# Kernel tuning notes

Hardware: AMD Instinct MI355X
Metric: run time of the kernel (lower is better)

The kernel has to match this reference:

```python
import jax, jax.numpy as jnp
import numpy as np

NLAT, NLON = 64, 64
CIN = 512
HEADS = 8


def _cc_weights(n):
    # Clenshaw-Curtis quadrature weights on [-1, 1] for nodes cos(k*pi/(n-1)),
    # as used by torch-harmonics for the 'equiangular' grid. Weights sum to 2.
    N = n - 1
    theta = np.pi * np.arange(n) / N
    m = N // 2
    j = np.arange(1, m + 1)
    b = np.where(2 * j == N, 1.0, 2.0)
    S = (b / (4.0 * j ** 2 - 1.0))[None, :] * np.cos(2.0 * j[None, :] * theta[:, None])
    w = 1.0 - S.sum(axis=1)
    c = np.full(n, 2.0)
    c[0] = 1.0
    c[-1] = 1.0
    return c * w / N


def _log_quad_weights(nlat, nlon):
    # _precompute_latitudes flips nodes/weights; then 2*pi*w/nlon tiled over lon.
    w = _cc_weights(nlat)[::-1].copy()
    qw = 2.0 * np.pi * w / nlon                       # (nlat,)
    qw = np.tile(qw[:, None], (1, nlon)).reshape(-1)  # (nlat*nlon,)
    return jnp.asarray(np.log(qw), dtype=jnp.float32)


def setup_inputs() -> dict:
    key = jax.random.key(0)
    ks = jax.random.split(key, 5)
    s_qkv = float(np.sqrt(3.0 / CIN))   # scale for q/k/v 1x1-conv weights
    s_proj = float(np.sqrt(3.0 / CIN))  # out_channels == CIN
    u = lambda k, sh, s: jax.random.uniform(k, sh, jnp.float32, -s, s)
    return dict(
        query=jax.random.normal(ks[0], (1, CIN, NLAT, NLON), jnp.float32),
        q_w=u(ks[1], (CIN, CIN), s_qkv), q_b=jnp.zeros((CIN,), jnp.float32),
        k_w=u(ks[2], (CIN, CIN), s_qkv), k_b=jnp.zeros((CIN,), jnp.float32),
        v_w=u(ks[3], (CIN, CIN), s_qkv), v_b=jnp.zeros((CIN,), jnp.float32),
        p_w=u(ks[4], (CIN, CIN), s_proj), p_b=jnp.zeros((CIN,), jnp.float32),
        log_quad_weights=_log_quad_weights(NLAT, NLON),
    )


def reference(query, q_w, q_b, k_w, k_b, v_w, v_b, p_w, p_b, log_quad_weights):
    B, C, H, W = query.shape
    hd = C // HEADS  # head dim (k_channels == out_channels == in_channels)

    def proj_tokens(x, w, b):
        # 1x1 conv == channel matmul, then split heads and flatten H*W tokens
        y = jnp.einsum('bihw,oi->bohw', x, w) + b[None, :, None, None]
        return y.reshape(B, HEADS, -1, H, W).transpose(0, 1, 3, 4, 2).reshape(B, HEADS, H * W, -1)

    q = proj_tokens(query, q_w, q_b)  # (B, heads, HW, hd)
    k = proj_tokens(query, k_w, k_b)  # self-attention: key/value default to query
    v = proj_tokens(query, v_w, v_b)

    scale = 1.0 / jnp.sqrt(jnp.asarray(hd, dtype=q.dtype))
    # additive log-quadrature bias over keys (broadcast over batch/head/query)
    logits = jnp.einsum('bhqd,bhkd->bhqk', q, k) * scale + log_quad_weights[None, None, None, :]
    attn = jax.nn.softmax(logits, axis=-1)
    out = jnp.einsum('bhqk,bhkd->bhqd', attn, v)          # (B, heads, HW, hd)
    out = out.transpose(0, 1, 3, 2).reshape(B, HEADS * hd, H, W)
    return jnp.einsum('bihw,oi->bohw', out, p_w) + p_b[None, :, None, None]
```

## Files before the change

kernel.cpp:

```cpp
#include <hip/hip_runtime.h>

typedef unsigned short u16;
typedef unsigned int u32;
typedef __bf16 bf16x8 __attribute__((ext_vector_type(8)));
typedef float f32x4 __attribute__((ext_vector_type(4)));
typedef unsigned short u16x4 __attribute__((ext_vector_type(4)));

#define LOG2E 1.4426950408889634f

#if __has_builtin(__builtin_amdgcn_exp2f)
#define EXP2F(x) __builtin_amdgcn_exp2f(x)
#else
#define EXP2F(x) exp2f(x)
#endif

__device__ __forceinline__ u16 f2bf(float f) {
    union { float f; u32 u; } a; a.f = f;
    u32 u = a.u;
    u += 0x7FFFu + ((u >> 16) & 1u);
    return (u16)(u >> 16);
}
__device__ __forceinline__ bf16x8 ldg8(const u16* p) {
    return *reinterpret_cast<const bf16x8*>(p);
}
#if __has_builtin(__builtin_amdgcn_cvt_pk_bf16_f32)
__device__ __forceinline__ u32 pack2(float a, float b) {
    auto r = __builtin_amdgcn_cvt_pk_bf16_f32(a, b);
    return __builtin_bit_cast(u32, r);
}
#else
__device__ __forceinline__ u32 pack2(float a, float b) {
    u32 ua = __float_as_uint(a) + 0x8000u;
    u32 ub = __float_as_uint(b) + 0x8000u;
    return __builtin_amdgcn_perm(ub, ua, 0x07060302);
}
#endif
__device__ __forceinline__ void async16(const void* g, void* l) {
    __builtin_amdgcn_global_load_lds(
        (const __attribute__((address_space(1))) u32*)g,
        (__attribute__((address_space(3))) u32*)l, 16, 0, 0);
}

#define MFMA16(a, b, c) __builtin_amdgcn_mfma_f32_16x16x32_bf16((a), (b), (c), 0, 0, 0)

__global__ __launch_bounds__(256) void prep(const float* __restrict__ X,
                                            u16* __restrict__ Xt,
                                            const float* __restrict__ s0,
                                            const float* __restrict__ s1,
                                            const float* __restrict__ s2,
                                            const float* __restrict__ s3,
                                            u16* __restrict__ Wqkv,
                                            u16* __restrict__ Wp,
                                            const float* __restrict__ lqw,
                                            float* __restrict__ lqw2g) {
    __shared__ u16 tile[64][65];
    const int tid = threadIdx.x;
    const int y = blockIdx.y;

    if (y < 8) {
        const int t0 = blockIdx.x * 64;
        const int c0 = y * 64;
#pragma unroll
        for (int i = 0; i < 16; ++i) {
            int idx = tid + i * 256;
            int r = idx >> 6, cc = idx & 63;
            tile[r][cc] = f2bf(X[(size_t)(c0 + r) * 4096 + t0 + cc]);
        }
        __syncthreads();
#pragma unroll
        for (int i = 0; i < 16; ++i) {
            int idx = tid + i * 256;
            int tr = idx >> 6, cc = idx & 63;
            Xt[(size_t)(t0 + tr) * 512 + c0 + cc] = tile[cc][tr];
        }
    } else if (y < 12) {
        const int m = y - 8;
        const float* s = (m == 0) ? s0 : (m == 1) ? s1 : (m == 2) ? s2 : s3;
        u16* d = (m == 3) ? Wp : Wqkv + (size_t)m * 262144;
#pragma unroll
        for (int j = 0; j < 4; ++j) {
            int i = blockIdx.x * 1024 + j * 256 + tid;
            float4 v = reinterpret_cast<const float4*>(s)[i];
            u16x4 o;
            o[0] = f2bf(v.x); o[1] = f2bf(v.y); o[2] = f2bf(v.z); o[3] = f2bf(v.w);
            reinterpret_cast<u16x4*>(d)[i] = o;
        }
    } else {
        if (blockIdx.x < 4) {
            int i = blockIdx.x * 256 + tid;
            float4 v = reinterpret_cast<const float4*>(lqw)[i];
            v.x *= LOG2E; v.y *= LOG2E; v.z *= LOG2E; v.w *= LOG2E;
            reinterpret_cast<float4*>(lqw2g)[i] = v;
        }
    }
}

__global__ __launch_bounds__(512, 2) void qkv_gemm(const u16* __restrict__ Wqkv,
                                                   const u16* __restrict__ Xt,
                                                   const float* __restrict__ qb,
                                                   const float* __restrict__ kb,
                                                   const float* __restrict__ vb,
                                                   u16* __restrict__ Qt,
                                                   u16* __restrict__ Kt,
                                                   u16* __restrict__ Vp) {
    __shared__ __align__(16) u16 Al[2][128 * 32];
    __shared__ __align__(16) u16 Bl[2][128 * 32];

    const int tid = threadIdx.x;
    const int w = tid >> 6, lane = tid & 63;
    const int quad = lane >> 4, lm = lane & 15;
    const int wm = w & 1, wn = w >> 1;
    const int n0 = blockIdx.x * 128;
    const int my = blockIdx.y;
    const int m0 = my * 128;

    const int arow = lane >> 2;
    const int sch = (lane & 3) ^ ((lane >> 3) & 3);
    const u16* agp = Wqkv + (size_t)(m0 + w * 16 + arow) * 512 + sch * 8;
    const u16* bgp = Xt + (size_t)(n0 + w * 16 + arow) * 512 + sch * 8;

    async16(agp, &Al[0][w * 16 * 32]);
    async16(bgp, &Bl[0][w * 16 * 32]);
    agp += 32; bgp += 32;

    const int FOFF = lm * 64 + ((quad ^ ((lm >> 1) & 3)) << 4);

    f32x4 acc[4][2];
#pragma unroll
    for (int mt = 0; mt < 4; ++mt)
#pragma unroll
        for (int bt = 0; bt < 2; ++bt) acc[mt][bt] = (f32x4){0.f, 0.f, 0.f, 0.f};

    __syncthreads();

    for (int s = 0; s < 16; ++s) {
        const int buf = s & 1;
        if (s < 15) {
            async16(agp, &Al[buf ^ 1][w * 16 * 32]);
            async16(bgp, &Bl[buf ^ 1][w * 16 * 32]);
            agp += 32; bgp += 32;
        }
        const char* Ab = (const char*)&Al[buf][0];
        const char* Bb = (const char*)&Bl[buf][0];
        bf16x8 af[4], bfr[2];
#pragma unroll
        for (int mt = 0; mt < 4; ++mt)
            af[mt] = *(const bf16x8*)(Ab + wm * 4096 + mt * 1024 + FOFF);
#pragma unroll
        for (int bt = 0; bt < 2; ++bt)
            bfr[bt] = *(const bf16x8*)(Bb + wn * 2048 + bt * 1024 + FOFF);
#pragma unroll
        for (int mt = 0; mt < 4; ++mt)
#pragma unroll
            for (int bt = 0; bt < 2; ++bt)
                acc[mt][bt] = MFMA16(af[mt], bfr[bt], acc[mt][bt]);
        __syncthreads();
    }

    const int mat = my >> 2;
    const float* bias = (mat == 0) ? qb : (mat == 1) ? kb : vb;
    const int chbase = (my & 3) * 128 + wm * 64 + quad * 4;

    if (mat < 2) {
        u16* out = mat ? Kt : Qt;
        const float sc = mat ? 1.0f : 0.125f * LOG2E;
#pragma unroll
        for (int mt = 0; mt < 4; ++mt) {
            const int ch = chbase + mt * 16;
            float4 bv = *(const float4*)(bias + ch);
            float bvf[4] = {bv.x, bv.y, bv.z, bv.w};
#pragma unroll
            for (int bt = 0; bt < 2; ++bt) {
                int tok = n0 + wn * 32 + bt * 16 + lm;
                u16x4 pk;
#pragma unroll
                for (int r = 0; r < 4; ++r)
                    pk[r] = f2bf((acc[mt][bt][r] + bvf[r]) * sc);
                *(u16x4*)(out + (size_t)tok * 512 + ch) = pk;
            }
        }
    } else {
#pragma unroll
        for (int mt = 0; mt < 4; ++mt) {
            const int ch = chbase + mt * 16;
            float4 bv = *(const float4*)(bias + ch);
            float bvf[4] = {bv.x, bv.y, bv.z, bv.w};
#pragma unroll
            for (int bt = 0; bt < 2; ++bt) {
                int g = bt * 16 + lm;
                int col = n0 + wn * 32 + 8 * ((g >> 2) & 3) + 4 * ((g >> 4) & 1) + (g & 3);
#pragma unroll
                for (int r = 0; r < 4; ++r)
                    Vp[(size_t)(ch + r) * 4096 + col] = f2bf(acc[mt][bt][r] + bvf[r]);
            }
        }
    }
}

__global__ __launch_bounds__(256, 2) void out_gemm(const u16* __restrict__ Wp,
                                                   const u16* __restrict__ Ot,
                                                   const float* __restrict__ pb,
                                                   float* __restrict__ out) {
    __shared__ __align__(16) u16 Al[2][128 * 32];
    __shared__ __align__(16) u16 Bl[2][64 * 32];

    const int tid = threadIdx.x;
    const int w = tid >> 6, lane = tid & 63;
    const int quad = lane >> 4, lm = lane & 15;
    const int wm = w & 1, wn = w >> 1;
    const int n0 = blockIdx.x * 64;
    const int m0 = blockIdx.y * 128;

    const int arow = lane >> 2;
    const int sch = (lane & 3) ^ ((lane >> 3) & 3);
    const u16* agp0 = Wp + (size_t)(m0 + w * 16 + arow) * 512 + sch * 8;
    const u16* agp1 = agp0 + (size_t)64 * 512;
    const u16* bgp = Ot + (size_t)(n0 + w * 16 + arow) * 512 + sch * 8;

    async16(agp0, &Al[0][w * 16 * 32]);
    async16(agp1, &Al[0][(64 + w * 16) * 32]);
    async16(bgp, &Bl[0][w * 16 * 32]);
    agp0 += 32; agp1 += 32; bgp += 32;

    const int FOFF = lm * 64 + ((quad ^ ((lm >> 1) & 3)) << 4);

    f32x4 acc[4][2];
#pragma unroll
    for (int mt = 0; mt < 4; ++mt)
#pragma unroll
        for (int bt = 0; bt < 2; ++bt) acc[mt][bt] = (f32x4){0.f, 0.f, 0.f, 0.f};

    __syncthreads();

    for (int s = 0; s < 16; ++s) {
        const int buf = s & 1;
        if (s < 15) {
            async16(agp0, &Al[buf ^ 1][w * 16 * 32]);
            async16(agp1, &Al[buf ^ 1][(64 + w * 16) * 32]);
            async16(bgp, &Bl[buf ^ 1][w * 16 * 32]);
            agp0 += 32; agp1 += 32; bgp += 32;
        }
        const char* Ab = (const char*)&Al[buf][0];
        const char* Bb = (const char*)&Bl[buf][0];
        bf16x8 af[4], bfr[2];
#pragma unroll
        for (int mt = 0; mt < 4; ++mt)
            af[mt] = *(const bf16x8*)(Ab + wm * 4096 + mt * 1024 + FOFF);
#pragma unroll
        for (int bt = 0; bt < 2; ++bt)
            bfr[bt] = *(const bf16x8*)(Bb + wn * 2048 + bt * 1024 + FOFF);
#pragma unroll
        for (int mt = 0; mt < 4; ++mt)
#pragma unroll
            for (int bt = 0; bt < 2; ++bt)
                acc[mt][bt] = MFMA16(af[mt], bfr[bt], acc[mt][bt]);
        __syncthreads();
    }

#pragma unroll
    for (int mt = 0; mt < 4; ++mt) {
        const int ch = m0 + wm * 64 + mt * 16 + quad * 4;
        float4 bv = *(const float4*)(pb + ch);
        float bvf[4] = {bv.x, bv.y, bv.z, bv.w};
#pragma unroll
        for (int bt = 0; bt < 2; ++bt) {
            int tok = n0 + wn * 32 + bt * 16 + lm;
#pragma unroll
            for (int r = 0; r < 4; ++r)
                out[(size_t)(ch + r) * 4096 + tok] = acc[mt][bt][r] + bvf[r];
        }
    }
}

#define WAITVM(N) asm volatile("s_waitcnt vmcnt(" #N ")" ::: "memory")

__global__ __launch_bounds__(256, 2) void flash_attn(const u16* __restrict__ Qt,
                                                     const u16* __restrict__ Kt,
                                                     const u16* __restrict__ Vp,
                                                     const float* __restrict__ lqw2g,
                                                     u16* __restrict__ Ot) {
    __shared__ __align__(16) char smem[65536];

    const int tid = threadIdx.x;
    const int w = tid >> 6, lane = tid & 63;
    const int quad = lane >> 4, lm = lane & 15;
    const int bid = blockIdx.x;
    const int h = bid & 7, hq = h * 64;
    const int q0 = (bid >> 3) * 64;
    const int kstart = w * 1024;

    char* kvw = smem + w * 8192;

    const int srow = lane >> 3;
    const int schunk = (lane & 7) ^ srow;
    const u16* kg = Kt + (size_t)(kstart + srow) * 512 + hq + schunk * 8;

    const u16* vp = Vp + (size_t)(hq + lm) * 4096 + kstart + quad * 8;

    bf16x8 bq0[4], bq1[4];
#pragma unroll
    for (int s = 0; s < 4; ++s) {
        const u16* qb = Qt + (size_t)(q0 + s * 16 + lm) * 512 + hq + quad * 8;
        bq0[s] = ldg8(qb);
        bq1[s] = ldg8(qb + 32);
    }

    f32x4 breg0 = *(const f32x4*)(lqw2g + kstart + quad * 4);
    f32x4 breg1 = *(const f32x4*)(lqw2g + kstart + 16 + quad * 4);
    const float* bptr = lqw2g + kstart + 32 + quad * 4;

    const int A0 = lm * 128 + ((quad ^ (lm & 7)) << 4);
    const int A1 = A0 ^ 64;

#define STAGEK(DST)                                                            \
    {                                                                          \
        char* nb = (DST);                                                      \
        async16(kg, nb);                                                       \
        async16(kg + 8 * 512, nb + 1024);                                      \
        async16(kg + 16 * 512, nb + 2048);                                     \
        async16(kg + 24 * 512, nb + 3072);                                     \
        kg += 32 * 512;                                                        \
    }

    STAGEK(kvw)
    STAGEK(kvw + 4096)

    union { u32 u[4]; bf16x8 v; } onesu;
    onesu.u[0] = onesu.u[1] = onesu.u[2] = onesu.u[3] = 0x3F803F80u;
    const bf16x8 onesv = onesu.v;

    f32x4 acc_o[4][4];
#pragma unroll
    for (int mt = 0; mt < 4; ++mt)
#pragma unroll
        for (int s = 0; s < 4; ++s) acc_o[mt][s] = (f32x4){0.f, 0.f, 0.f, 0.f};
    f32x4 acc_l[4];
#pragma unroll
    for (int s = 0; s < 4; ++s) acc_l[s] = (f32x4){0.f, 0.f, 0.f, 0.f};

    union { u32 u[4]; bf16x8 v; } pb_[4];
    bf16x8 pv0, pv1, pv2, pv3;
    int bufsel = 0;

#define BODY(WN, DOBIAS, DOSTAGE, DOPV)                                        \
    {                                                                          \
        WAITVM(WN);                                                            \
        bf16x8 nv0 = ldg8(vp);                                                 \
        bf16x8 nv1 = ldg8(vp + (size_t)16 * 4096);                             \
        bf16x8 nv2 = ldg8(vp + (size_t)32 * 4096);                             \
        bf16x8 nv3 = ldg8(vp + (size_t)48 * 4096);                             \
        vp += 32;                                                              \
        const char* Kb = kvw + bufsel;                                         \
        bf16x8 k00 = *(const bf16x8*)(Kb + A0);                                \
        bf16x8 k01 = *(const bf16x8*)(Kb + A1);                                \
        bf16x8 k10 = *(const bf16x8*)(Kb + 2048 + A0);                         \
        bf16x8 k11 = *(const bf16x8*)(Kb + 2048 + A1);                         \
        if (DOPV) {                                                            \
            _Pragma("unroll")                                                  \
            for (int s = 0; s < 4; ++s) {                                      \
                acc_o[0][s] = MFMA16(pv0, pb_[s].v, acc_o[0][s]);              \
                acc_o[1][s] = MFMA16(pv1, pb_[s].v, acc_o[1][s]);              \
                acc_o[2][s] = MFMA16(pv2, pb_[s].v, acc_o[2][s]);              \
                acc_o[3][s] = MFMA16(pv3, pb_[s].v, acc_o[3][s]);              \
                acc_l[s] = MFMA16(onesv, pb_[s].v, acc_l[s]);                  \
            }                                                                  \
        }                                                                      \
        _Pragma("unroll")                                                      \
        for (int s = 0; s < 4; ++s) {                                          \
            f32x4 a = MFMA16(k00, bq0[s], breg0);                              \
            a = MFMA16(k01, bq1[s], a);                                        \
            pb_[s].u[0] = pack2(EXP2F(a[0]), EXP2F(a[1]));                     \
            pb_[s].u[1] = pack2(EXP2F(a[2]), EXP2F(a[3]));                     \
        }                                                                      \
        _Pragma("unroll")                                                      \
        for (int s = 0; s < 4; ++s) {                                          \
            f32x4 c = MFMA16(k10, bq0[s], breg1);                              \
            c = MFMA16(k11, bq1[s], c);                                        \
            pb_[s].u[2] = pack2(EXP2F(c[0]), EXP2F(c[1]));                     \
            pb_[s].u[3] = pack2(EXP2F(c[2]), EXP2F(c[3]));                     \
        }                                                                      \
        if (DOBIAS) {                                                          \
            breg0 = *(const f32x4*)(bptr);                                     \
            breg1 = *(const f32x4*)(bptr + 16);                                \
            bptr += 32;                                                        \
        }                                                                      \
        pv0 = nv0; pv1 = nv1; pv2 = nv2; pv3 = nv3;                            \
        if (DOSTAGE) STAGEK(kvw + bufsel)                                      \
        bufsel ^= 4096;                                                        \
    }

    BODY(4, true, true, false)
    for (int t = 1; t < 30; ++t)
        BODY(10, true, true, true)
    BODY(10, true, false, true)
    BODY(6, false, false, true)

#undef BODY
#undef STAGEK

#pragma unroll
    for (int s = 0; s < 4; ++s) {
        acc_o[0][s] = MFMA16(pv0, pb_[s].v, acc_o[0][s]);
        acc_o[1][s] = MFMA16(pv1, pb_[s].v, acc_o[1][s]);
        acc_o[2][s] = MFMA16(pv2, pb_[s].v, acc_o[2][s]);
        acc_o[3][s] = MFMA16(pv3, pb_[s].v, acc_o[3][s]);
        acc_l[s] = MFMA16(onesv, pb_[s].v, acc_l[s]);
    }

    __syncthreads();
    float* mbuf = (float*)smem;
    if (w != 0) {
        float* ob = mbuf + (w - 1) * 4096;
#pragma unroll
        for (int s = 0; s < 4; ++s) {
            const int r = s * 16 + lm;
#pragma unroll
            for (int mt = 0; mt < 4; ++mt) {
                const int sl = (mt * 4 + quad) ^ lm;
                *(f32x4*)(ob + r * 64 + sl * 4) = acc_o[mt][s];
            }
        }
        if (quad == 0) {
#pragma unroll
            for (int s = 0; s < 4; ++s)
                mbuf[12288 + (w - 1) * 64 + s * 16 + lm] = acc_l[s][0];
        }
    }
    __syncthreads();
    if (w != 0) return;

#pragma unroll
    for (int s = 0; s < 4; ++s) {
        const int r = s * 16 + lm;
        float lsum = acc_l[s][0];
#pragma unroll
        for (int p = 0; p < 3; ++p)
            lsum += mbuf[12288 + p * 64 + r];
        const float inv = 1.0f / lsum;
#pragma unroll
        for (int mt = 0; mt < 4; ++mt) {
            const int sl = (mt * 4 + quad) ^ lm;
            f32x4 o = acc_o[mt][s];
#pragma unroll
            for (int p = 0; p < 3; ++p)
                o += *(const f32x4*)(mbuf + p * 4096 + r * 64 + sl * 4);
            u16x4 pkv;
#pragma unroll
            for (int r2 = 0; r2 < 4; ++r2)
                pkv[r2] = f2bf(o[r2] * inv);
            *reinterpret_cast<u16x4*>(Ot + (size_t)(q0 + r) * 512 +
                                      hq + mt * 16 + quad * 4) = pkv;
        }
    }
}

extern "C" void kernel_launch(void* const* d_in, const int* in_sizes, int n_in,
                              void* d_out, int out_size, void* d_ws, size_t ws_size,
                              hipStream_t stream) {
    (void)in_sizes; (void)n_in; (void)out_size; (void)ws_size;
    const float* X   = (const float*)d_in[0];
    const float* qw  = (const float*)d_in[1];
    const float* qb  = (const float*)d_in[2];
    const float* kw  = (const float*)d_in[3];
    const float* kb  = (const float*)d_in[4];
    const float* vw  = (const float*)d_in[5];
    const float* vb  = (const float*)d_in[6];
    const float* pw  = (const float*)d_in[7];
    const float* pb  = (const float*)d_in[8];
    const float* lqw = (const float*)d_in[9];

    const size_t E = (size_t)4096 * 512;
    const size_t WE = (size_t)512 * 512;
    u16* Xt    = (u16*)d_ws;
    u16* Qt    = Xt + E;
    u16* Kt    = Qt + E;
    u16* Vp    = Kt + E;
    u16* Wqkv  = Vp + E;
    u16* Wp    = Wqkv + 3 * WE;
    float* lqw2g = (float*)(Wp + WE);
    u16* Ot    = Xt;

    prep<<<dim3(64, 13), dim3(256), 0, stream>>>(X, Xt, qw, kw, vw, pw,
                                                 Wqkv, Wp, lqw, lqw2g);
    qkv_gemm<<<dim3(32, 12), dim3(512), 0, stream>>>(Wqkv, Xt, qb, kb, vb, Qt, Kt, Vp);
    flash_attn<<<dim3(512), dim3(256), 0, stream>>>(Qt, Kt, Vp, lqw2g, Ot);
    out_gemm<<<dim3(64, 4), dim3(256), 0, stream>>>(Wp, Ot, pb, (float*)d_out);
}
```

Baseline: 83.11 us.

## Store V in a per-lane fragment image so attention loads are contiguous

Result: faster. 77.39 us (-6.9%).

```diff
diff --git a/kernel.cpp b/kernel.cpp
--- a/kernel.cpp
+++ b/kernel.cpp
@@ -102,7 +102,7 @@
                                                    const float* __restrict__ vb,
                                                    u16* __restrict__ Qt,
                                                    u16* __restrict__ Kt,
-                                                   u16* __restrict__ Vp) {
+                                                   u16* __restrict__ Vimg) {
     __shared__ __align__(16) u16 Al[2][128 * 32];
     __shared__ __align__(16) u16 Bl[2][128 * 32];
 
@@ -185,13 +185,21 @@
             const int ch = chbase + mt * 16;
             float4 bv = *(const float4*)(bias + ch);
             float bvf[4] = {bv.x, bv.y, bv.z, bv.w};
+            const int hh = ch >> 6;
+            const int D0 = ch & 63;
 #pragma unroll
             for (int bt = 0; bt < 2; ++bt) {
                 int g = bt * 16 + lm;
-                int col = n0 + wn * 32 + 8 * ((g >> 2) & 3) + 4 * ((g >> 4) & 1) + (g & 3);
-#pragma unroll
-                for (int r = 0; r < 4; ++r)
-                    Vp[(size_t)(ch + r) * 4096 + col] = f2bf(acc[mt][bt][r] + bvf[r]);
+                int key2 = 8 * ((g >> 2) & 3) + 4 * ((g >> 4) & 1) + (g & 3);
+                int t = (n0 >> 5) + wn;
+                int kc = key2 >> 3, ke = key2 & 7;
+                u16* vdst = Vimg + (size_t)(hh * 128 + t) * 2048 + ke;
+#pragma unroll
+                for (int r = 0; r < 4; ++r) {
+                    int D = D0 + r;
+                    int lane_i = kc * 16 + ((D >> 1) & 7) * 2 + (D & 1);
+                    vdst[(size_t)(D >> 4) * 512 + lane_i * 8] = f2bf(acc[mt][bt][r] + bvf[r]);
+                }
             }
         }
     }
@@ -276,7 +284,7 @@
 
 __global__ __launch_bounds__(256, 2) void flash_attn(const u16* __restrict__ Qt,
                                                      const u16* __restrict__ Kt,
-                                                     const u16* __restrict__ Vp,
+                                                     const u16* __restrict__ Vimg,
                                                      const float* __restrict__ lqw2g,
                                                      u16* __restrict__ Ot) {
     __shared__ __align__(16) char smem[65536];
@@ -295,7 +303,7 @@
     const int schunk = (lane & 7) ^ srow;
     const u16* kg = Kt + (size_t)(kstart + srow) * 512 + hq + schunk * 8;
 
-    const u16* vp = Vp + (size_t)(hq + lm) * 4096 + kstart + quad * 8;
+    const u16* vp = Vimg + (size_t)(h * 128 + w * 32) * 2048 + (size_t)lane * 8;
 
     bf16x8 bq0[4], bq1[4];
 #pragma unroll
@@ -346,10 +354,10 @@
     {                                                                          \
         WAITVM(WN);                                                            \
         bf16x8 nv0 = ldg8(vp);                                                 \
-        bf16x8 nv1 = ldg8(vp + (size_t)16 * 4096);                             \
-        bf16x8 nv2 = ldg8(vp + (size_t)32 * 4096);                             \
-        bf16x8 nv3 = ldg8(vp + (size_t)48 * 4096);                             \
-        vp += 32;                                                              \
+        bf16x8 nv1 = ldg8(vp + 512);                                           \
+        bf16x8 nv2 = ldg8(vp + 1024);                                          \
+        bf16x8 nv3 = ldg8(vp + 1536);                                          \
+        vp += 2048;                                                            \
         const char* Kb = kvw + bufsel;                                         \
         bf16x8 k00 = *(const bf16x8*)(Kb + A0);                                \
         bf16x8 k01 = *(const bf16x8*)(Kb + A1);                                \
@@ -392,8 +400,8 @@
     BODY(4, true, true, false)
     for (int t = 1; t < 30; ++t)
         BODY(10, true, true, true)
-    BODY(10, true, false, true)
-    BODY(6, false, false, true)
+    BODY(6, true, false, true)
+    BODY(2, false, false, true)
 
 #undef BODY
 #undef STAGEK
@@ -474,15 +482,15 @@
     u16* Xt    = (u16*)d_ws;
     u16* Qt    = Xt + E;
     u16* Kt    = Qt + E;
-    u16* Vp    = Kt + E;
-    u16* Wqkv  = Vp + E;
+    u16* Vimg  = Kt + E;
+    u16* Wqkv  = Vimg + E;
     u16* Wp    = Wqkv + 3 * WE;
     float* lqw2g = (float*)(Wp + WE);
     u16* Ot    = Xt;
 
     prep<<<dim3(64, 13), dim3(256), 0, stream>>>(X, Xt, qw, kw, vw, pw,
                                                  Wqkv, Wp, lqw, lqw2g);
-    qkv_gemm<<<dim3(32, 12), dim3(512), 0, stream>>>(Wqkv, Xt, qb, kb, vb, Qt, Kt, Vp);
-    flash_attn<<<dim3(512), dim3(256), 0, stream>>>(Qt, Kt, Vp, lqw2g, Ot);
+    qkv_gemm<<<dim3(32, 12), dim3(512), 0, stream>>>(Wqkv, Xt, qb, kb, vb, Qt, Kt, Vimg);
+    flash_attn<<<dim3(512), dim3(256), 0, stream>>>(Qt, Kt, Vimg, lqw2g, Ot);
     out_gemm<<<dim3(64, 4), dim3(256), 0, stream>>>(Wp, Ot, pb, (float*)d_out);
 }
```
